# Performance work log

Hardware: AMD Instinct MI355X
Metric: run time of the kernel (lower is better)

## Reference

```python
import jax, jax.numpy as jnp
import numpy as np

B, T, N, C, H = 64, 12, 1370, 8, 64

def setup_inputs() -> dict:
    key = jax.random.key(0)
    ks = jax.random.split(key, 7)
    s_ih = 1.0 / np.sqrt(H)
    inp = {
        "x": jax.random.normal(ks[0], (B, T, N, C), dtype=jnp.float32),
        # PyTorch nn.LSTM params, gate order (i, f, g, o)
        "W_ih": jax.random.uniform(ks[1], (4 * H, C), jnp.float32, -s_ih, s_ih),
        "W_hh": jax.random.uniform(ks[2], (4 * H, H), jnp.float32, -s_ih, s_ih),
        "b_ih": jax.random.uniform(ks[3], (4 * H,), jnp.float32, -s_ih, s_ih),
        "b_hh": jax.random.uniform(ks[4], (4 * H,), jnp.float32, -s_ih, s_ih),
        "W_fc": jax.random.uniform(ks[5], (C, H), jnp.float32, -s_ih, s_ih),
        "b_fc": jax.random.uniform(ks[6], (C,), jnp.float32, -s_ih, s_ih),
    }
    return inp

def reference(x, W_ih, W_hh, b_ih, b_hh, W_fc, b_fc):
    Bx, Tx, Nx, Cx = x.shape
    Hh = W_hh.shape[1]
    # (B, T, N, C) -> (B*N, T, C): shared-weight LSTM over all node sequences
    xr = jnp.transpose(x, (0, 2, 1, 3)).reshape(Bx * Nx, Tx, Cx)
    # Precompute input projections for all timesteps: (B*N, T, 4H)
    x_gates = jnp.einsum('btc,gc->btg', xr, W_ih) + b_ih
    # time-major for scan: (T, B*N, 4H)
    x_gates = jnp.moveaxis(x_gates, 1, 0)

    def step(carry, xg):
        h, c = carry
        gates = xg + h @ W_hh.T + b_hh  # (B*N, 4H)
        i, f, g, o = jnp.split(gates, 4, axis=-1)
        i = jax.nn.sigmoid(i)
        f = jax.nn.sigmoid(f)
        g = jnp.tanh(g)
        o = jax.nn.sigmoid(o)
        c = f * c + i * g
        h = o * jnp.tanh(c)
        return (h, c), None

    h0 = jnp.zeros((Bx * Nx, Hh), dtype=x.dtype)
    c0 = jnp.zeros((Bx * Nx, Hh), dtype=x.dtype)
    (h_last, _), _ = jax.lax.scan(step, (h0, c0), x_gates)

    y_flat = h_last @ W_fc.T + b_fc  # (B*N, C)
    return y_flat.reshape(Bx, Nx, Cx)
```

## Files before the change

### kernel.cpp

```cpp
#include <hip/hip_runtime.h>

#define T_ 12
#define N_ 1370
#define C_ 8
#define H_ 64
#define MSEQ 64
#define LDA 104

typedef __attribute__((ext_vector_type(8))) short short8;
typedef __attribute__((ext_vector_type(4))) float floatx4;
typedef __attribute__((ext_vector_type(2))) float floatx2;

__device__ __forceinline__ float sigmoid_f(float x) {
  return __builtin_amdgcn_rcpf(1.0f + __builtin_amdgcn_exp2f(x * -1.4426950408889634f));
}
__device__ __forceinline__ float tanh_f(float x) {
  float e = __builtin_amdgcn_exp2f(x * 2.8853900817779268f);
  return 1.0f - 2.0f * __builtin_amdgcn_rcpf(1.0f + e);
}
__device__ __forceinline__ short f2bf(float x) {
  unsigned u = __builtin_bit_cast(unsigned, x);
  u = (u + 0x7fffu + ((u >> 16) & 1u)) >> 16;
  return (short)u;
}
__device__ __forceinline__ short8 load_w8(const float* __restrict__ p) {
  short8 r;
#pragma unroll
  for (int j = 0; j < 8; ++j) r[j] = f2bf(p[j]);
  return r;
}

__global__ void __launch_bounds__(256) lstm_kernel(
    const float* __restrict__ x, const float* __restrict__ W_ih,
    const float* __restrict__ W_hh, const float* __restrict__ b_ih,
    const float* __restrict__ b_hh, const float* __restrict__ W_fc,
    const float* __restrict__ b_fc, float* __restrict__ out) {
  __shared__ short A[2][MSEQ][LDA];

  const int tid = threadIdx.x;
  const int wave = tid >> 6;
  const int lane = tid & 63;
  const int m16 = lane & 15;
  const int q = lane >> 4;
  const int blk = blockIdx.x;

  const int u = wave * 16 + m16;
  short8 bf[4][3];
  float bias[4];
#pragma unroll
  for (int g = 0; g < 4; ++g) {
    const int grow = g * 64 + u;
    const float* wr = W_hh + grow * 64;
    bf[g][0] = load_w8(wr + q * 8);
    bf[g][1] = load_w8(wr + 32 + q * 8);
    if (q == 0) {
      bf[g][2] = load_w8(W_ih + grow * 8);
    } else {
      short8 z = {0, 0, 0, 0, 0, 0, 0, 0};
      bf[g][2] = z;
    }
    bias[g] = b_ih[grow] + b_hh[grow];
  }

  const int xrow = tid >> 2;
  const int xcp = tid & 3;
  const int s0 = blk * MSEQ + xrow;
  const int bidx = s0 / N_;
  const int nidx = s0 - bidx * N_;
  const float* xptr = x + ((size_t)bidx * T_ * N_ + nidx) * C_ + xcp * 2;

  {
    int* Ai = (int*)A;
#pragma unroll
    for (int i = tid; i < (2 * MSEQ * LDA) / 2; i += 256) Ai[i] = 0;
  }
  __syncthreads();
  {
    floatx2 v = *(const floatx2*)(xptr);
    unsigned pk = (unsigned short)f2bf(v.x) |
                  ((unsigned)(unsigned short)f2bf(v.y) << 16);
    *(int*)&A[0][xrow][64 + xcp * 2] = pk;
  }
  __syncthreads();

  float cst[4][4];
#pragma unroll
  for (int mt = 0; mt < 4; ++mt)
#pragma unroll
    for (int r = 0; r < 4; ++r) cst[mt][r] = 0.0f;

  for (int t = 0; t < T_; ++t) {
    const int rb = t & 1, wb = rb ^ 1;
    short hreg[16];
#pragma unroll
    for (int mt = 0; mt < 4; ++mt) {
      const short* arow = &A[rb][mt * 16 + m16][0];
      short8 a0 = *(const short8*)(arow + q * 8);
      short8 a1 = *(const short8*)(arow + 32 + q * 8);
      short8 a2 = *(const short8*)(arow + 64 + q * 8);
      floatx4 gi = {bias[0], bias[0], bias[0], bias[0]};
      floatx4 gf = {bias[1], bias[1], bias[1], bias[1]};
      floatx4 gg = {bias[2], bias[2], bias[2], bias[2]};
      floatx4 go = {bias[3], bias[3], bias[3], bias[3]};
      gi = __builtin_amdgcn_mfma_f32_16x16x32_bf16(a0, bf[0][0], gi, 0, 0, 0);
      gf = __builtin_amdgcn_mfma_f32_16x16x32_bf16(a0, bf[1][0], gf, 0, 0, 0);
      gg = __builtin_amdgcn_mfma_f32_16x16x32_bf16(a0, bf[2][0], gg, 0, 0, 0);
      go = __builtin_amdgcn_mfma_f32_16x16x32_bf16(a0, bf[3][0], go, 0, 0, 0);
      gi = __builtin_amdgcn_mfma_f32_16x16x32_bf16(a1, bf[0][1], gi, 0, 0, 0);
      gf = __builtin_amdgcn_mfma_f32_16x16x32_bf16(a1, bf[1][1], gf, 0, 0, 0);
      gg = __builtin_amdgcn_mfma_f32_16x16x32_bf16(a1, bf[2][1], gg, 0, 0, 0);
      go = __builtin_amdgcn_mfma_f32_16x16x32_bf16(a1, bf[3][1], go, 0, 0, 0);
      gi = __builtin_amdgcn_mfma_f32_16x16x32_bf16(a2, bf[0][2], gi, 0, 0, 0);
      gf = __builtin_amdgcn_mfma_f32_16x16x32_bf16(a2, bf[1][2], gf, 0, 0, 0);
      gg = __builtin_amdgcn_mfma_f32_16x16x32_bf16(a2, bf[2][2], gg, 0, 0, 0);
      go = __builtin_amdgcn_mfma_f32_16x16x32_bf16(a2, bf[3][2], go, 0, 0, 0);
#pragma unroll
      for (int r = 0; r < 4; ++r) {
        float iv = sigmoid_f(gi[r]);
        float fv = sigmoid_f(gf[r]);
        float gv = tanh_f(gg[r]);
        float ov = sigmoid_f(go[r]);
        float cc = fv * cst[mt][r] + iv * gv;
        cst[mt][r] = cc;
        hreg[mt * 4 + r] = f2bf(ov * tanh_f(cc));
      }
    }
#pragma unroll
    for (int mt = 0; mt < 4; ++mt)
#pragma unroll
      for (int r = 0; r < 4; ++r)
        A[wb][mt * 16 + q * 4 + r][u] = hreg[mt * 4 + r];
    if (t + 1 < T_) {
      floatx2 v = *(const floatx2*)(xptr + (size_t)(t + 1) * (N_ * C_));
      unsigned pk = (unsigned short)f2bf(v.x) |
                    ((unsigned)(unsigned short)f2bf(v.y) << 16);
      *(int*)&A[wb][xrow][64 + xcp * 2] = pk;
    }
    __syncthreads();
  }

  short8 fb0, fb1;
  float fbias = 0.0f;
  if (m16 < 8) {
    const float* wr = W_fc + m16 * 64;
    fb0 = load_w8(wr + q * 8);
    fb1 = load_w8(wr + 32 + q * 8);
    fbias = b_fc[m16];
  } else {
    short8 z = {0, 0, 0, 0, 0, 0, 0, 0};
    fb0 = z;
    fb1 = z;
  }
  {
    const int mt = wave;
    const short* arow = &A[0][mt * 16 + m16][0];
    short8 a0 = *(const short8*)(arow + q * 8);
    short8 a1 = *(const short8*)(arow + 32 + q * 8);
    floatx4 acc = {fbias, fbias, fbias, fbias};
    acc = __builtin_amdgcn_mfma_f32_16x16x32_bf16(a0, fb0, acc, 0, 0, 0);
    acc = __builtin_amdgcn_mfma_f32_16x16x32_bf16(a1, fb1, acc, 0, 0, 0);
    if (m16 < 8) {
      const int srow = blk * MSEQ + mt * 16 + q * 4;
#pragma unroll
      for (int r = 0; r < 4; ++r) out[(srow + r) * 8 + m16] = acc[r];
    }
  }
}

extern "C" void kernel_launch(void* const* d_in, const int* in_sizes, int n_in,
                              void* d_out, int out_size, void* d_ws,
                              size_t ws_size, hipStream_t stream) {
  const float* x    = (const float*)d_in[0];
  const float* W_ih = (const float*)d_in[1];
  const float* W_hh = (const float*)d_in[2];
  const float* b_ih = (const float*)d_in[3];
  const float* b_hh = (const float*)d_in[4];
  const float* W_fc = (const float*)d_in[5];
  const float* b_fc = (const float*)d_in[6];
  float* out = (float*)d_out;
  hipLaunchKernelGGL(lstm_kernel, dim3(1370), dim3(256), 0, stream,
                     x, W_ih, W_hh, b_ih, b_hh, W_fc, b_fc, out);
}
```

Before: 187.0 us.

## Halve sequences per block, fold activation scales into weights, pack bf16 stores

Each block now processes 32 sequences instead of 64 and the grid doubles, so each wave handles two row tiles instead of four. The -log2e and 2log2e factors for sigmoid and tanh are folded into the bf16 weights and biases, which removes multiplies from the recurrent activation path. Hidden states are converted with a packed bf16 instruction and written straight to shared memory. The trade-off is that per-block weight loading and conversion are amortised over fewer sequences, and the final FC wave count is reduced.

```diff
diff --git a/kernel.cpp b/kernel.cpp
--- a/kernel.cpp
+++ b/kernel.cpp
@@ -4,29 +4,31 @@
 #define N_ 1370
 #define C_ 8
 #define H_ 64
-#define MSEQ 64
-#define LDA 104
+#define MSEQ 32
+#define NT 2
+#define LDA 88
+#define NBLK 2740
 
 typedef __attribute__((ext_vector_type(8))) short short8;
 typedef __attribute__((ext_vector_type(4))) float floatx4;
-typedef __attribute__((ext_vector_type(2))) float floatx2;
 
-__device__ __forceinline__ float sigmoid_f(float x) {
-  return __builtin_amdgcn_rcpf(1.0f + __builtin_amdgcn_exp2f(x * -1.4426950408889634f));
-}
-__device__ __forceinline__ float tanh_f(float x) {
-  float e = __builtin_amdgcn_exp2f(x * 2.8853900817779268f);
-  return 1.0f - 2.0f * __builtin_amdgcn_rcpf(1.0f + e);
-}
+#define NLOG2E -1.4426950408889634f
+#define TLOG2E 2.8853901817779268f
+
 __device__ __forceinline__ short f2bf(float x) {
   unsigned u = __builtin_bit_cast(unsigned, x);
   u = (u + 0x7fffu + ((u >> 16) & 1u)) >> 16;
   return (short)u;
 }
-__device__ __forceinline__ short8 load_w8(const float* __restrict__ p) {
+__device__ __forceinline__ unsigned pk_bf16(float a, float b) {
+  unsigned r;
+  asm("v_cvt_pk_bf16_f32 %0, %1, %2" : "=v"(r) : "v"(a), "v"(b));
+  return r;
+}
+__device__ __forceinline__ short8 load_w8s(const float* __restrict__ p, float s) {
   short8 r;
 #pragma unroll
-  for (int j = 0; j < 8; ++j) r[j] = f2bf(p[j]);
+  for (int j = 0; j < 8; ++j) r[j] = f2bf(p[j] * s);
   return r;
 }
 
@@ -49,51 +51,47 @@
   float bias[4];
 #pragma unroll
   for (int g = 0; g < 4; ++g) {
+    const float sg = (g == 2) ? TLOG2E : NLOG2E;
     const int grow = g * 64 + u;
     const float* wr = W_hh + grow * 64;
-    bf[g][0] = load_w8(wr + q * 8);
-    bf[g][1] = load_w8(wr + 32 + q * 8);
+    bf[g][0] = load_w8s(wr + q * 8, sg);
+    bf[g][1] = load_w8s(wr + 32 + q * 8, sg);
     if (q == 0) {
-      bf[g][2] = load_w8(W_ih + grow * 8);
+      bf[g][2] = load_w8s(W_ih + grow * 8, sg);
     } else {
       short8 z = {0, 0, 0, 0, 0, 0, 0, 0};
       bf[g][2] = z;
     }
-    bias[g] = b_ih[grow] + b_hh[grow];
+    bias[g] = sg * (b_ih[grow] + b_hh[grow]);
   }
 
-  const int xrow = tid >> 2;
-  const int xcp = tid & 3;
+  const int xrow = tid >> 3;
+  const int xcol = tid & 7;
   const int s0 = blk * MSEQ + xrow;
   const int bidx = s0 / N_;
   const int nidx = s0 - bidx * N_;
-  const float* xptr = x + ((size_t)bidx * T_ * N_ + nidx) * C_ + xcp * 2;
+  const float* xptr = x + ((size_t)bidx * T_ * N_ + nidx) * C_ + xcol;
 
   {
     int* Ai = (int*)A;
 #pragma unroll
-    for (int i = tid; i < (2 * MSEQ * LDA) / 2; i += 256) Ai[i] = 0;
+    for (int i = 0; i < (2 * MSEQ * LDA) / (2 * 256); ++i)
+      Ai[i * 256 + tid] = 0;
   }
   __syncthreads();
-  {
-    floatx2 v = *(const floatx2*)(xptr);
-    unsigned pk = (unsigned short)f2bf(v.x) |
-                  ((unsigned)(unsigned short)f2bf(v.y) << 16);
-    *(int*)&A[0][xrow][64 + xcp * 2] = pk;
-  }
+  A[0][xrow][64 + xcol] = f2bf(*xptr);
   __syncthreads();
 
-  float cst[4][4];
+  float cst[NT][4];
 #pragma unroll
-  for (int mt = 0; mt < 4; ++mt)
+  for (int mt = 0; mt < NT; ++mt)
 #pragma unroll
     for (int r = 0; r < 4; ++r) cst[mt][r] = 0.0f;
 
   for (int t = 0; t < T_; ++t) {
     const int rb = t & 1, wb = rb ^ 1;
-    short hreg[16];
 #pragma unroll
-    for (int mt = 0; mt < 4; ++mt) {
+    for (int mt = 0; mt < NT; ++mt) {
       const short* arow = &A[rb][mt * 16 + m16][0];
       short8 a0 = *(const short8*)(arow + q * 8);
       short8 a1 = *(const short8*)(arow + 32 + q * 8);
@@ -114,44 +112,45 @@
       gf = __builtin_amdgcn_mfma_f32_16x16x32_bf16(a2, bf[1][2], gf, 0, 0, 0);
       gg = __builtin_amdgcn_mfma_f32_16x16x32_bf16(a2, bf[2][2], gg, 0, 0, 0);
       go = __builtin_amdgcn_mfma_f32_16x16x32_bf16(a2, bf[3][2], go, 0, 0, 0);
+      float hv[4];
 #pragma unroll
       for (int r = 0; r < 4; ++r) {
-        float iv = sigmoid_f(gi[r]);
-        float fv = sigmoid_f(gf[r]);
-        float gv = tanh_f(gg[r]);
-        float ov = sigmoid_f(go[r]);
-        float cc = fv * cst[mt][r] + iv * gv;
+        float iv = __builtin_amdgcn_rcpf(1.0f + __builtin_amdgcn_exp2f(gi[r]));
+        float fv = __builtin_amdgcn_rcpf(1.0f + __builtin_amdgcn_exp2f(gf[r]));
+        float gv = fmaf(-2.0f, __builtin_amdgcn_rcpf(1.0f + __builtin_amdgcn_exp2f(gg[r])), 1.0f);
+        float ov = __builtin_amdgcn_rcpf(1.0f + __builtin_amdgcn_exp2f(go[r]));
+        float cc = fmaf(fv, cst[mt][r], iv * gv);
         cst[mt][r] = cc;
-        hreg[mt * 4 + r] = f2bf(ov * tanh_f(cc));
+        float tc = fmaf(-2.0f, __builtin_amdgcn_rcpf(1.0f + __builtin_amdgcn_exp2f(cc * TLOG2E)), 1.0f);
+        hv[r] = ov * tc;
       }
+      unsigned p01 = pk_bf16(hv[0], hv[1]);
+      unsigned p23 = pk_bf16(hv[2], hv[3]);
+      const int rbase = mt * 16 + q * 4;
+      A[wb][rbase + 0][u] = (short)p01;
+      A[wb][rbase + 1][u] = (short)(p01 >> 16);
+      A[wb][rbase + 2][u] = (short)p23;
+      A[wb][rbase + 3][u] = (short)(p23 >> 16);
     }
-#pragma unroll
-    for (int mt = 0; mt < 4; ++mt)
-#pragma unroll
-      for (int r = 0; r < 4; ++r)
-        A[wb][mt * 16 + q * 4 + r][u] = hreg[mt * 4 + r];
     if (t + 1 < T_) {
-      floatx2 v = *(const floatx2*)(xptr + (size_t)(t + 1) * (N_ * C_));
-      unsigned pk = (unsigned short)f2bf(v.x) |
-                    ((unsigned)(unsigned short)f2bf(v.y) << 16);
-      *(int*)&A[wb][xrow][64 + xcp * 2] = pk;
+      A[wb][xrow][64 + xcol] = f2bf(xptr[(size_t)(t + 1) * (N_ * C_)]);
     }
     __syncthreads();
   }
 
-  short8 fb0, fb1;
-  float fbias = 0.0f;
-  if (m16 < 8) {
-    const float* wr = W_fc + m16 * 64;
-    fb0 = load_w8(wr + q * 8);
-    fb1 = load_w8(wr + 32 + q * 8);
-    fbias = b_fc[m16];
-  } else {
-    short8 z = {0, 0, 0, 0, 0, 0, 0, 0};
-    fb0 = z;
-    fb1 = z;
-  }
-  {
+  if (wave < NT) {
+    short8 fb0, fb1;
+    float fbias = 0.0f;
+    if (m16 < 8) {
+      const float* wr = W_fc + m16 * 64;
+      fb0 = load_w8s(wr + q * 8, 1.0f);
+      fb1 = load_w8s(wr + 32 + q * 8, 1.0f);
+      fbias = b_fc[m16];
+    } else {
+      short8 z = {0, 0, 0, 0, 0, 0, 0, 0};
+      fb0 = z;
+      fb1 = z;
+    }
     const int mt = wave;
     const short* arow = &A[0][mt * 16 + m16][0];
     short8 a0 = *(const short8*)(arow + q * 8);
@@ -178,6 +177,6 @@
   const float* W_fc = (const float*)d_in[5];
   const float* b_fc = (const float*)d_in[6];
   float* out = (float*)d_out;
-  hipLaunchKernelGGL(lstm_kernel, dim3(1370), dim3(256), 0, stream,
+  hipLaunchKernelGGL(lstm_kernel, dim3(NBLK), dim3(256), 0, stream,
                      x, W_ih, W_hh, b_ih, b_hh, W_fc, b_fc, out);
 }
```

New measurement: 181.3 us. 1.03x faster.
